# Performance work log

Measured on AMD Instinct MI355X. Metric: run time of the kernel, lower is better.

## Reference

```python
import jax, jax.numpy as jnp
import numpy as np

T, H, E, I, K = 2048, 2048, 32, 768, 8  # tokens, hidden, experts, moe_intermediate, top_k


def setup_inputs() -> dict:
    key = jax.random.key(0)
    k1, k2, k3, k4, k5 = jax.random.split(key, 5)
    return {
        "hidden_states": jax.random.normal(k1, (T, H), dtype=jnp.float32),
        "w_gate": jax.random.normal(k2, (H, E), dtype=jnp.float32) * 0.02,
        "w_gate_proj": jax.random.normal(k3, (E, H, I), dtype=jnp.float32) * 0.02,
        "w_up_proj": jax.random.normal(k4, (E, H, I), dtype=jnp.float32) * 0.02,
        "w_down_proj": jax.random.normal(k5, (E, I, H), dtype=jnp.float32) * 0.02,
    }


def reference(hidden_states, w_gate, w_gate_proj, w_up_proj, w_down_proj):
    # Router: softmax over expert logits, top-k, renormalize (RoutingMethodType.Renormalize,
    # norm_topk_prob=True in Qwen3 MoE config).
    x = hidden_states                                  # [T, H]
    n_tok = x.shape[0]
    logits = x @ w_gate                                # [T, E]
    probs = jax.nn.softmax(logits, axis=-1)            # [T, E]
    topk_w, topk_idx = jax.lax.top_k(probs, K)         # [T, K]
    topk_w = topk_w / jnp.sum(topk_w, axis=-1, keepdims=True)
    # Sparse combine weights [T, E]: zero except the K selected experts per token.
    combine = jnp.zeros_like(probs).at[jnp.arange(n_tok)[:, None], topk_idx].set(topk_w)

    # Expert SwiGLU MLPs (gate/up/down), computed for all experts then combined with
    # the sparse weights -- mathematically identical to top-k dispatch + grouped GEMM.
    g = jnp.einsum('th,ehi->tei', x, w_gate_proj)      # [T, E, I]
    u = jnp.einsum('th,ehi->tei', x, w_up_proj)        # [T, E, I]
    act = jax.nn.silu(g) * u                           # [T, E, I]
    # Combine expert outputs without materializing [T, E, H].
    out = jnp.einsum('tei,eih,te->th', act, w_down_proj, combine)  # [T, H]
    return out
```

## Files before the change

kernel.cpp:

```cpp
#include <hip/hip_runtime.h>

#define T_TOK 2048
#define HD    2048
#define NE    32
#define ID    768
#define TOPK  8
#define NPAIR (T_TOK * TOPK)

typedef short bf16x8 __attribute__((ext_vector_type(8)));
typedef float f32x4  __attribute__((ext_vector_type(4)));

__device__ inline unsigned short f2bf(float f) {
    unsigned u = __builtin_bit_cast(unsigned, f);
    u += 0x7FFF + ((u >> 16) & 1);
    return (unsigned short)(u >> 16);
}

__device__ inline void gload16(const void* g, void* l) {
    __builtin_amdgcn_global_load_lds(
        (const __attribute__((address_space(1))) unsigned*)g,
        (__attribute__((address_space(3))) unsigned*)l, 16, 0, 0);
}

__device__ inline int xcd_swz(int x, int nblk) {
    int chunk = nblk >> 3;
    return (x & 7) * chunk + (x >> 3);
}

__global__ void cvt_x(const float* __restrict__ x, unsigned short* __restrict__ x16) {
    int i = blockIdx.x * blockDim.x + threadIdx.x;
    const float4* src = (const float4*)x + (size_t)i * 2;
    float4 a = src[0], b = src[1];
    uint4 r;
    r.x = (unsigned)f2bf(a.x) | ((unsigned)f2bf(a.y) << 16);
    r.y = (unsigned)f2bf(a.z) | ((unsigned)f2bf(a.w) << 16);
    r.z = (unsigned)f2bf(b.x) | ((unsigned)f2bf(b.y) << 16);
    r.w = (unsigned)f2bf(b.z) | ((unsigned)f2bf(b.w) << 16);
    *(uint4*)(x16 + (size_t)i * 8) = r;
}

__global__ void transpose_cvt(const float* __restrict__ in, unsigned short* __restrict__ out,
                              int R, int C) {
    int e = blockIdx.z;
    int r0 = blockIdx.y * 64, c0 = blockIdx.x * 64;
    const float* src = in + (size_t)e * R * C;
    unsigned short* dst = out + (size_t)e * R * C;
    __shared__ float tile[64][65];
    int tid = threadIdx.x;
    #pragma unroll
    for (int j = 0; j < 4; ++j) {
        int idx = tid + 256 * j;
        int rr = idx >> 4, c4 = (idx & 15) * 4;
        float4 v = *(const float4*)&src[(size_t)(r0 + rr) * C + c0 + c4];
        tile[rr][c4] = v.x; tile[rr][c4 + 1] = v.y; tile[rr][c4 + 2] = v.z; tile[rr][c4 + 3] = v.w;
    }
    __syncthreads();
    #pragma unroll
    for (int j = 0; j < 2; ++j) {
        int idx = tid + 256 * j;
        int cc = idx >> 3, r8 = (idx & 7) * 8;
        uint4 o;
        unsigned* po = (unsigned*)&o;
        #pragma unroll
        for (int q = 0; q < 4; ++q)
            po[q] = (unsigned)f2bf(tile[r8 + 2 * q][cc]) |
                    ((unsigned)f2bf(tile[r8 + 2 * q + 1][cc]) << 16);
        *(uint4*)&dst[(size_t)(c0 + cc) * R + r0 + r8] = o;
    }
}

__global__ void router_kernel(const float* __restrict__ x, const float* __restrict__ wg,
                              int* __restrict__ topk_idx, float* __restrict__ topk_w,
                              int* __restrict__ counts) {
    int t = blockIdx.x;
    int tid = threadIdx.x;
    int e = tid & 31, seg = tid >> 5;
    const float* xr = x + (size_t)t * HD + seg * 256;
    const float* wp = wg + (size_t)(seg * 256) * NE + e;
    float acc = 0.f;
    #pragma unroll 4
    for (int j = 0; j < 256; ++j) acc += xr[j] * wp[j * NE];
    __shared__ float part[8][33];
    __shared__ float lg[32];
    part[seg][e] = acc;
    __syncthreads();
    if (tid < 32) {
        float s = 0.f;
        #pragma unroll
        for (int g = 0; g < 8; ++g) s += part[g][tid];
        lg[tid] = s;
    }
    __syncthreads();
    if (tid == 0) {
        float m = lg[0];
        for (int i = 1; i < 32; ++i) m = fmaxf(m, lg[i]);
        for (int i = 0; i < 32; ++i) lg[i] = __expf(lg[i] - m);
        int   idxs[TOPK]; float wv[TOPK]; float wsum = 0.f;
        #pragma unroll
        for (int k = 0; k < TOPK; ++k) {
            float best = -1.f; int bi = 0;
            for (int i = 0; i < 32; ++i) if (lg[i] > best) { best = lg[i]; bi = i; }
            idxs[k] = bi; wv[k] = best; wsum += best; lg[bi] = -1.f;
        }
        #pragma unroll
        for (int k = 0; k < TOPK; ++k) {
            topk_idx[t * TOPK + k] = idxs[k];
            topk_w[t * TOPK + k]   = wv[k] / wsum;
            atomicAdd(&counts[idxs[k]], 1);
        }
    }
}

__global__ void offsets_kernel(const int* __restrict__ counts, int* __restrict__ offsets,
                               int* __restrict__ cursor) {
    if (threadIdx.x == 0 && blockIdx.x == 0) {
        int run = 0;
        for (int e = 0; e < NE; ++e) { offsets[e] = run; cursor[e] = run; run += counts[e]; }
    }
}

__global__ void scatter_kernel(const int* __restrict__ topk_idx, int* __restrict__ cursor,
                               int* __restrict__ token_list) {
    int i = blockIdx.x * 256 + threadIdx.x;
    int e = topk_idx[i];
    int pos = atomicAdd(&cursor[e], 1);
    token_list[pos] = i;
}

__global__ __launch_bounds__(256, 2)
void gemm1_kernel(const unsigned short* __restrict__ X16,
                  const unsigned short* __restrict__ WG, const unsigned short* __restrict__ WU,
                  const int* __restrict__ token_list, const int* __restrict__ counts,
                  const int* __restrict__ offsets, unsigned short* __restrict__ act16) {
    int f = xcd_swz(blockIdx.x, 32 * 6 * 16);
    int e = f / 96, rem = f % 96;
    int it = rem / 16, tt = rem % 16;
    int ne = counts[e];
    int row0 = tt * 128;
    if (row0 >= ne) return;
    int base = offsets[e];
    int i0 = it * 128;

    __shared__ __align__(16) unsigned short As[128 * 64];
    __shared__ __align__(16) unsigned short Bg[128 * 64];
    __shared__ __align__(16) unsigned short Bu[128 * 64];
    __shared__ int rowTok[128];

    int tid = threadIdx.x;
    if (tid < 128) {
        int r = row0 + tid;
        rowTok[tid] = (r < ne) ? (token_list[base + r] >> 3) : 0;
    }
    __syncthreads();

    int lane = tid & 63, w = tid >> 6;
    int sub = lane & 7, lrow = lane >> 3;

    const unsigned short* aP[4]; const unsigned short* gP[4]; const unsigned short* uP[4];
    #pragma unroll
    for (int c = 0; c < 4; ++c) {
        int q = w * 4 + c;
        int r = q * 8 + lrow;
        int chunk = (sub ^ (r & 7)) * 8;
        aP[c] = X16 + (size_t)rowTok[r] * HD + chunk;
        gP[c] = WG + ((size_t)e * ID + i0 + r) * HD + chunk;
        uP[c] = WU + ((size_t)e * ID + i0 + r) * HD + chunk;
    }

    f32x4 accg[4][4], accu[4][4];
    #pragma unroll
    for (int m = 0; m < 4; ++m)
        #pragma unroll
        for (int n = 0; n < 4; ++n) {
            f32x4 z = {0.f, 0.f, 0.f, 0.f};
            accg[m][n] = z; accu[m][n] = z;
        }

    int wm = w >> 1, wn = w & 1, l15 = lane & 15, lhi = lane >> 4;
    const bf16x8* Af = (const bf16x8*)As;
    const bf16x8* Gf = (const bf16x8*)Bg;
    const bf16x8* Uf = (const bf16x8*)Bu;

    for (int k0 = 0; k0 < HD; k0 += 64) {
        #pragma unroll
        for (int c = 0; c < 4; ++c) {
            int q = w * 4 + c;
            gload16(aP[c] + k0, (char*)As + q * 1024);
            gload16(gP[c] + k0, (char*)Bg + q * 1024);
            gload16(uP[c] + k0, (char*)Bu + q * 1024);
        }
        __syncthreads();
        #pragma unroll
        for (int ks = 0; ks < 2; ++ks) {
            int cc = ks * 4 + lhi;
            bf16x8 a[4], bg[4], bu[4];
            #pragma unroll
            for (int m = 0; m < 4; ++m) { int r = wm * 64 + m * 16 + l15; a[m] = Af[r * 8 + (cc ^ (r & 7))]; }
            #pragma unroll
            for (int n = 0; n < 4; ++n) {
                int r = wn * 64 + n * 16 + l15;
                bg[n] = Gf[r * 8 + (cc ^ (r & 7))];
                bu[n] = Uf[r * 8 + (cc ^ (r & 7))];
            }
            #pragma unroll
            for (int m = 0; m < 4; ++m)
                #pragma unroll
                for (int n = 0; n < 4; ++n) {
                    accg[m][n] = __builtin_amdgcn_mfma_f32_16x16x32_bf16(a[m], bg[n], accg[m][n], 0, 0, 0);
                    accu[m][n] = __builtin_amdgcn_mfma_f32_16x16x32_bf16(a[m], bu[n], accu[m][n], 0, 0, 0);
                }
        }
        __syncthreads();
    }

    #pragma unroll
    for (int m = 0; m < 4; ++m) {
        int rb = wm * 64 + m * 16 + lhi * 4;
        #pragma unroll
        for (int q = 0; q < 4; ++q) {
            int r = rb + q;
            if (row0 + r < ne) {
                size_t orow = (size_t)(base + row0 + r) * ID + i0 + wn * 64;
                #pragma unroll
                for (int n = 0; n < 4; ++n) {
                    float g = accg[m][n][q], uu = accu[m][n][q];
                    float a = g / (1.f + __expf(-g)) * uu;
                    act16[orow + n * 16 + l15] = f2bf(a);
                }
            }
        }
    }
}

__global__ __launch_bounds__(256, 2)
void gemm2_kernel(const unsigned short* __restrict__ act16, const unsigned short* __restrict__ WD,
                  const int* __restrict__ token_list, const int* __restrict__ counts,
                  const int* __restrict__ offsets, const float* __restrict__ topk_w,
                  float* __restrict__ out) {
    int f = xcd_swz(blockIdx.x, 32 * 8 * 16);
    int e = f / 128, rem = f % 128;
    int ht = rem / 16, tt = rem % 16;
    int ne = counts[e];
    int row0 = tt * 128;
    if (row0 >= ne) return;
    int base = offsets[e];
    int h0 = ht * 256;

    __shared__ __align__(16) unsigned short As[128 * 64];
    __shared__ __align__(16) unsigned short Bs[256 * 64];
    __shared__ int   rowTok[128];
    __shared__ float rowW[128];

    int tid = threadIdx.x;
    if (tid < 128) {
        int r = row0 + tid;
        if (r < ne) { int v = token_list[base + r]; rowTok[tid] = v >> 3; rowW[tid] = topk_w[v]; }
        else        { rowTok[tid] = 0;              rowW[tid] = 0.f; }
    }
    __syncthreads();

    int lane = tid & 63, w = tid >> 6;
    int sub = lane & 7, lrow = lane >> 3;

    const unsigned short* aP[4]; const unsigned short* bP[8];
    #pragma unroll
    for (int c = 0; c < 4; ++c) {
        int q = w * 4 + c;
        int r = q * 8 + lrow;
        int chunk = (sub ^ (r & 7)) * 8;
        int pr = base + row0 + r;
        if (pr > NPAIR - 1) pr = NPAIR - 1;
        aP[c] = act16 + (size_t)pr * ID + chunk;
    }
    #pragma unroll
    for (int c = 0; c < 8; ++c) {
        int q = w * 8 + c;
        int r = q * 8 + lrow;
        int chunk = (sub ^ (r & 7)) * 8;
        bP[c] = WD + ((size_t)e * HD + h0 + r) * ID + chunk;
    }

    f32x4 acc[4][8];
    #pragma unroll
    for (int m = 0; m < 4; ++m)
        #pragma unroll
        for (int n = 0; n < 8; ++n) { f32x4 z = {0.f, 0.f, 0.f, 0.f}; acc[m][n] = z; }

    int wm = w >> 1, wn = w & 1, l15 = lane & 15, lhi = lane >> 4;
    const bf16x8* Af = (const bf16x8*)As;
    const bf16x8* Bf = (const bf16x8*)Bs;

    for (int k0 = 0; k0 < ID; k0 += 64) {
        #pragma unroll
        for (int c = 0; c < 4; ++c) {
            int q = w * 4 + c;
            gload16(aP[c] + k0, (char*)As + q * 1024);
        }
        #pragma unroll
        for (int c = 0; c < 8; ++c) {
            int q = w * 8 + c;
            gload16(bP[c] + k0, (char*)Bs + q * 1024);
        }
        __syncthreads();
        #pragma unroll
        for (int ks = 0; ks < 2; ++ks) {
            int cc = ks * 4 + lhi;
            bf16x8 a[4], b[8];
            #pragma unroll
            for (int m = 0; m < 4; ++m) { int r = wm * 64 + m * 16 + l15; a[m] = Af[r * 8 + (cc ^ (r & 7))]; }
            #pragma unroll
            for (int n = 0; n < 8; ++n) { int r = wn * 128 + n * 16 + l15; b[n] = Bf[r * 8 + (cc ^ (r & 7))]; }
            #pragma unroll
            for (int m = 0; m < 4; ++m)
                #pragma unroll
                for (int n = 0; n < 8; ++n)
                    acc[m][n] = __builtin_amdgcn_mfma_f32_16x16x32_bf16(a[m], b[n], acc[m][n], 0, 0, 0);
        }
        __syncthreads();
    }

    #pragma unroll
    for (int m = 0; m < 4; ++m) {
        int rb = wm * 64 + m * 16 + lhi * 4;
        #pragma unroll
        for (int q = 0; q < 4; ++q) {
            int r = rb + q;
            if (row0 + r < ne) {
                int tok = rowTok[r];
                float wgt = rowW[r];
                float* orow = out + (size_t)tok * HD + h0 + wn * 128;
                #pragma unroll
                for (int n = 0; n < 8; ++n)
                    atomicAdd(&orow[n * 16 + l15], acc[m][n][q] * wgt);
            }
        }
    }
}

extern "C" void kernel_launch(void* const* d_in, const int* in_sizes, int n_in,
                              void* d_out, int out_size, void* d_ws, size_t ws_size,
                              hipStream_t stream) {
    const float* x   = (const float*)d_in[0];
    const float* wg  = (const float*)d_in[1];
    const float* wgp = (const float*)d_in[2];
    const float* wup = (const float*)d_in[3];
    const float* wdp = (const float*)d_in[4];
    float* out = (float*)d_out;

    char* ws = (char*)d_ws;
    size_t off = 0;
    unsigned short* X16   = (unsigned short*)(ws + off); off += (size_t)T_TOK * HD * 2;
    unsigned short* act16 = (unsigned short*)(ws + off); off += (size_t)NPAIR * ID * 2;
    int*   topk_idx   = (int*)(ws + off);   off += NPAIR * 4;
    float* topk_w     = (float*)(ws + off); off += NPAIR * 4;
    int*   token_list = (int*)(ws + off);   off += NPAIR * 4;
    int*   counts     = (int*)(ws + off);   off += 256;
    int*   offsets    = (int*)(ws + off);   off += 256;
    int*   cursor     = (int*)(ws + off);   off += 256;
    unsigned short* WG = (unsigned short*)(ws + off); off += (size_t)NE * ID * HD * 2;
    unsigned short* WU = (unsigned short*)(ws + off); off += (size_t)NE * ID * HD * 2;
    unsigned short* WD = (unsigned short*)(ws + off); off += (size_t)NE * HD * ID * 2;
    (void)in_sizes; (void)n_in; (void)out_size; (void)ws_size;

    hipMemsetAsync(counts, 0, 256, stream);
    hipMemsetAsync(d_out, 0, (size_t)T_TOK * HD * 4, stream);

    cvt_x<<<T_TOK * HD / (256 * 8), 256, 0, stream>>>(x, X16);
    router_kernel<<<T_TOK, 256, 0, stream>>>(x, wg, topk_idx, topk_w, counts);
    offsets_kernel<<<1, 64, 0, stream>>>(counts, offsets, cursor);
    scatter_kernel<<<NPAIR / 256, 256, 0, stream>>>(topk_idx, cursor, token_list);

    transpose_cvt<<<dim3(ID / 64, HD / 64, NE), 256, 0, stream>>>(wgp, WG, HD, ID);
    transpose_cvt<<<dim3(ID / 64, HD / 64, NE), 256, 0, stream>>>(wup, WU, HD, ID);
    transpose_cvt<<<dim3(HD / 64, ID / 64, NE), 256, 0, stream>>>(wdp, WD, ID, HD);

    gemm1_kernel<<<32 * 6 * 16, 256, 0, stream>>>(X16, WG, WU, token_list, counts, offsets, act16);
    gemm2_kernel<<<32 * 8 * 16, 256, 0, stream>>>(act16, WD, token_list, counts, offsets, topk_w, out);
}
```

Baseline: 685.8 us.

## Build compact per-expert tile list to launch only occupied GEMM tiles

Replaces the fixed grid of experts × 16 token tiles, in which most blocks exit early, with a precomputed tile table (expert, start, count) sized for at most 160 tiles. Each expert's segment is padded to a multiple of 128 rows, so gemm1 writes full tiles and gemm2 reads act16 without clamping. The aim is to cut the launch and early-exit overhead of idle blocks. The XCD swizzle is dropped, which may hurt L2 locality of weight tiles, and MAXT=160 assumes the padded tile count never exceeds 160.

```diff
diff --git a/kernel.cpp b/kernel.cpp
--- a/kernel.cpp
+++ b/kernel.cpp
@@ -6,6 +6,7 @@
 #define ID    768
 #define TOPK  8
 #define NPAIR (T_TOK * TOPK)
+#define MAXT  160
 
 typedef short bf16x8 __attribute__((ext_vector_type(8)));
 typedef float f32x4  __attribute__((ext_vector_type(4)));
@@ -20,11 +21,6 @@
     __builtin_amdgcn_global_load_lds(
         (const __attribute__((address_space(1))) unsigned*)g,
         (__attribute__((address_space(3))) unsigned*)l, 16, 0, 0);
-}
-
-__device__ inline int xcd_swz(int x, int nblk) {
-    int chunk = nblk >> 3;
-    return (x & 7) * chunk + (x >> 3);
 }
 
 __global__ void cvt_x(const float* __restrict__ x, unsigned short* __restrict__ x16) {
@@ -111,11 +107,24 @@
     }
 }
 
-__global__ void offsets_kernel(const int* __restrict__ counts, int* __restrict__ offsets,
-                               int* __restrict__ cursor) {
+__global__ void build_tiles(const int* __restrict__ counts, int* __restrict__ cursor,
+                            int* __restrict__ tE, int* __restrict__ tStart,
+                            int* __restrict__ tCnt) {
     if (threadIdx.x == 0 && blockIdx.x == 0) {
-        int run = 0;
-        for (int e = 0; e < NE; ++e) { offsets[e] = run; cursor[e] = run; run += counts[e]; }
+        int run = 0, nt = 0;
+        for (int e = 0; e < NE; ++e) {
+            cursor[e] = run;
+            int c = counts[e];
+            int nte = (c + 127) >> 7;
+            for (int j = 0; j < nte; ++j) {
+                tE[nt] = e;
+                tStart[nt] = run + j * 128;
+                tCnt[nt] = (c - j * 128 < 128) ? (c - j * 128) : 128;
+                ++nt;
+            }
+            run += nte * 128;
+        }
+        for (; nt < MAXT; ++nt) { tE[nt] = -1; tStart[nt] = 0; tCnt[nt] = 0; }
     }
 }
 
@@ -130,15 +139,13 @@
 __global__ __launch_bounds__(256, 2)
 void gemm1_kernel(const unsigned short* __restrict__ X16,
                   const unsigned short* __restrict__ WG, const unsigned short* __restrict__ WU,
-                  const int* __restrict__ token_list, const int* __restrict__ counts,
-                  const int* __restrict__ offsets, unsigned short* __restrict__ act16) {
-    int f = xcd_swz(blockIdx.x, 32 * 6 * 16);
-    int e = f / 96, rem = f % 96;
-    int it = rem / 16, tt = rem % 16;
-    int ne = counts[e];
-    int row0 = tt * 128;
-    if (row0 >= ne) return;
-    int base = offsets[e];
+                  const int* __restrict__ token_list,
+                  const int* __restrict__ tE, const int* __restrict__ tStart,
+                  const int* __restrict__ tCnt, unsigned short* __restrict__ act16) {
+    int tile = blockIdx.x / 6, it = blockIdx.x % 6;
+    int e = tE[tile];
+    if (e < 0) return;
+    int start = tStart[tile], cnt = tCnt[tile];
     int i0 = it * 128;
 
     __shared__ __align__(16) unsigned short As[128 * 64];
@@ -147,10 +154,8 @@
     __shared__ int rowTok[128];
 
     int tid = threadIdx.x;
-    if (tid < 128) {
-        int r = row0 + tid;
-        rowTok[tid] = (r < ne) ? (token_list[base + r] >> 3) : 0;
-    }
+    if (tid < 128)
+        rowTok[tid] = (tid < cnt) ? (token_list[start + tid] >> 3) : 0;
     __syncthreads();
 
     int lane = tid & 63, w = tid >> 6;
@@ -219,14 +224,12 @@
         #pragma unroll
         for (int q = 0; q < 4; ++q) {
             int r = rb + q;
-            if (row0 + r < ne) {
-                size_t orow = (size_t)(base + row0 + r) * ID + i0 + wn * 64;
-                #pragma unroll
-                for (int n = 0; n < 4; ++n) {
-                    float g = accg[m][n][q], uu = accu[m][n][q];
-                    float a = g / (1.f + __expf(-g)) * uu;
-                    act16[orow + n * 16 + l15] = f2bf(a);
-                }
+            size_t orow = (size_t)(start + r) * ID + i0 + wn * 64;
+            #pragma unroll
+            for (int n = 0; n < 4; ++n) {
+                float g = accg[m][n][q], uu = accu[m][n][q];
+                float a = g / (1.f + __expf(-g)) * uu;
+                act16[orow + n * 16 + l15] = f2bf(a);
             }
         }
     }
@@ -234,16 +237,14 @@
 
 __global__ __launch_bounds__(256, 2)
 void gemm2_kernel(const unsigned short* __restrict__ act16, const unsigned short* __restrict__ WD,
-                  const int* __restrict__ token_list, const int* __restrict__ counts,
-                  const int* __restrict__ offsets, const float* __restrict__ topk_w,
+                  const int* __restrict__ token_list,
+                  const int* __restrict__ tE, const int* __restrict__ tStart,
+                  const int* __restrict__ tCnt, const float* __restrict__ topk_w,
                   float* __restrict__ out) {
-    int f = xcd_swz(blockIdx.x, 32 * 8 * 16);
-    int e = f / 128, rem = f % 128;
-    int ht = rem / 16, tt = rem % 16;
-    int ne = counts[e];
-    int row0 = tt * 128;
-    if (row0 >= ne) return;
-    int base = offsets[e];
+    int tile = blockIdx.x / 8, ht = blockIdx.x % 8;
+    int e = tE[tile];
+    if (e < 0) return;
+    int start = tStart[tile], cnt = tCnt[tile];
     int h0 = ht * 256;
 
     __shared__ __align__(16) unsigned short As[128 * 64];
@@ -253,9 +254,8 @@
 
     int tid = threadIdx.x;
     if (tid < 128) {
-        int r = row0 + tid;
-        if (r < ne) { int v = token_list[base + r]; rowTok[tid] = v >> 3; rowW[tid] = topk_w[v]; }
-        else        { rowTok[tid] = 0;              rowW[tid] = 0.f; }
+        if (tid < cnt) { int v = token_list[start + tid]; rowTok[tid] = v >> 3; rowW[tid] = topk_w[v]; }
+        else           { rowTok[tid] = 0;                 rowW[tid] = 0.f; }
     }
     __syncthreads();
 
@@ -268,9 +268,7 @@
         int q = w * 4 + c;
         int r = q * 8 + lrow;
         int chunk = (sub ^ (r & 7)) * 8;
-        int pr = base + row0 + r;
-        if (pr > NPAIR - 1) pr = NPAIR - 1;
-        aP[c] = act16 + (size_t)pr * ID + chunk;
+        aP[c] = act16 + (size_t)(start + r) * ID + chunk;
     }
     #pragma unroll
     for (int c = 0; c < 8; ++c) {
@@ -325,7 +323,7 @@
         #pragma unroll
         for (int q = 0; q < 4; ++q) {
             int r = rb + q;
-            if (row0 + r < ne) {
+            if (r < cnt) {
                 int tok = rowTok[r];
                 float wgt = rowW[r];
                 float* orow = out + (size_t)tok * HD + h0 + wn * 128;
@@ -350,13 +348,16 @@
     char* ws = (char*)d_ws;
     size_t off = 0;
     unsigned short* X16   = (unsigned short*)(ws + off); off += (size_t)T_TOK * HD * 2;
-    unsigned short* act16 = (unsigned short*)(ws + off); off += (size_t)NPAIR * ID * 2;
+    unsigned short* act16 = (unsigned short*)(ws + off); off += (size_t)MAXT * 128 * ID * 2;
     int*   topk_idx   = (int*)(ws + off);   off += NPAIR * 4;
     float* topk_w     = (float*)(ws + off); off += NPAIR * 4;
-    int*   token_list = (int*)(ws + off);   off += NPAIR * 4;
+    int*   token_list = (int*)(ws + off);   off += MAXT * 128 * 4;
     int*   counts     = (int*)(ws + off);   off += 256;
-    int*   offsets    = (int*)(ws + off);   off += 256;
     int*   cursor     = (int*)(ws + off);   off += 256;
+    int*   tE         = (int*)(ws + off);   off += MAXT * 4;
+    int*   tStart     = (int*)(ws + off);   off += MAXT * 4;
+    int*   tCnt       = (int*)(ws + off);   off += MAXT * 4;
+    off = (off + 255) & ~(size_t)255;
     unsigned short* WG = (unsigned short*)(ws + off); off += (size_t)NE * ID * HD * 2;
     unsigned short* WU = (unsigned short*)(ws + off); off += (size_t)NE * ID * HD * 2;
     unsigned short* WD = (unsigned short*)(ws + off); off += (size_t)NE * HD * ID * 2;
@@ -367,13 +368,13 @@
 
     cvt_x<<<T_TOK * HD / (256 * 8), 256, 0, stream>>>(x, X16);
     router_kernel<<<T_TOK, 256, 0, stream>>>(x, wg, topk_idx, topk_w, counts);
-    offsets_kernel<<<1, 64, 0, stream>>>(counts, offsets, cursor);
+    build_tiles<<<1, 64, 0, stream>>>(counts, cursor, tE, tStart, tCnt);
     scatter_kernel<<<NPAIR / 256, 256, 0, stream>>>(topk_idx, cursor, token_list);
 
     transpose_cvt<<<dim3(ID / 64, HD / 64, NE), 256, 0, stream>>>(wgp, WG, HD, ID);
     transpose_cvt<<<dim3(ID / 64, HD / 64, NE), 256, 0, stream>>>(wup, WU, HD, ID);
     transpose_cvt<<<dim3(HD / 64, ID / 64, NE), 256, 0, stream>>>(wdp, WD, ID, HD);
 
-    gemm1_kernel<<<32 * 6 * 16, 256, 0, stream>>>(X16, WG, WU, token_list, counts, offsets, act16);
-    gemm2_kernel<<<32 * 8 * 16, 256, 0, stream>>>(act16, WD, token_list, counts, offsets, topk_w, out);
-}
+    gemm1_kernel<<<MAXT * 6, 256, 0, stream>>>(X16, WG, WU, token_list, tE, tStart, tCnt, act16);
+    gemm2_kernel<<<MAXT * 8, 256, 0, stream>>>(act16, WD, token_list, tE, tStart, tCnt, topk_w, out);
+}
```

Measured after the change: 656.4 us. -4.3%, faster.
